# Optimization experiments

Hardware: AMD Instinct MI355X
Metric: run time of the kernel (lower is better)

The kernel has to match this reference:

```python
import jax, jax.numpy as jnp
import numpy as np

N_ITEMS = 30000
D = 128            # embedding_dim
F = D // 2 + 1     # freq_dim = 65
RAW_IMG = 1024
RAW_TXT = 768


def setup_inputs() -> dict:
    key = jax.random.key(0)
    ks = jax.random.split(key, 13)
    return {
        "image_embeds": jax.random.normal(ks[0], (N_ITEMS, D), jnp.float32),
        "text_embeds": jax.random.normal(ks[1], (N_ITEMS, D), jnp.float32),
        "image_table": jax.random.normal(ks[2], (N_ITEMS, RAW_IMG), jnp.float32),
        "text_table": jax.random.normal(ks[3], (N_ITEMS, RAW_TXT), jnp.float32),
        "W_img": jax.random.normal(ks[4], (RAW_IMG, D), jnp.float32) * 0.02,
        "b_img": jax.random.normal(ks[5], (D,), jnp.float32) * 0.02,
        "W_txt": jax.random.normal(ks[6], (RAW_TXT, D), jnp.float32) * 0.02,
        "b_txt": jax.random.normal(ks[7], (D,), jnp.float32) * 0.02,
        "avrf_img": jax.random.normal(ks[8], (F,), jnp.float32),
        "avrf_txt": jax.random.normal(ks[9], (F,), jnp.float32),
        "avg_R": jax.random.normal(ks[10], (F,), jnp.float32),
        "psi": jax.random.normal(ks[11], (F,), jnp.float32) * 0.1,
        "lambda_weights": jnp.array([0.6, 0.4], jnp.float32),
    }


def reference(image_embeds, text_embeds, image_table, text_table,
              W_img, b_img, W_txt, b_txt,
              avrf_img, avrf_txt, avg_R, psi, lambda_weights):
    # project full embedding tables: [N, raw] @ [raw, D] -> [N, D]
    proj_image = image_table @ W_img + b_img
    proj_txt = text_table @ W_txt + b_txt
    # per-row rFFT -> [N, F] complex
    img_fft = jnp.fft.rfft(proj_image, axis=1, norm="ortho")
    txt_fft = jnp.fft.rfft(proj_txt, axis=1, norm="ortho")
    # phase alignment rotation
    phi = avg_R * 0.5 + psi                      # [F]
    rot = jnp.exp(-1j * phi.astype(jnp.complex64))
    APC_img = img_fft * rot[None, :]
    APC_txt = txt_fft * jnp.conj(rot)[None, :]
    # AVRF (variance-ratio) masking -- torch forward uses the raw logit params
    img_vr = APC_img * avrf_img[None, :]
    txt_vr = APC_txt * avrf_txt[None, :]
    # IMCF: magnitude-squared coherence masking
    cross = APC_img * jnp.conj(APC_txt)
    msc = jnp.abs(cross) ** 2 / (jnp.abs(APC_img) ** 2 * jnp.abs(APC_txt) ** 2 + 1e-8)
    img_imcf = APC_img * msc
    txt_imcf = APC_txt * msc
    # softmax-weighted late fusion of the two filtered spectra
    lam = jax.nn.softmax(lambda_weights)
    img_late = lam[0] * img_vr + lam[1] * img_imcf
    txt_late = lam[0] * txt_vr + lam[1] * txt_imcf
    image_conv = jnp.fft.irfft(img_late, n=image_embeds.shape[1], axis=1, norm="ortho")
    text_conv = jnp.fft.irfft(txt_late, n=text_embeds.shape[1], axis=1, norm="ortho")
    return image_conv, text_conv
```

## Files before the change

kernel.cpp:

```cpp
#include <hip/hip_runtime.h>
#include <math.h>

typedef __bf16 bf16x8 __attribute__((ext_vector_type(8)));
typedef float f32x4 __attribute__((ext_vector_type(4)));
typedef unsigned short u16;
typedef unsigned int u32;

#define S128 0.08838834764831845f
#define TWOPI_128 0.04908738521234052f
#define MROWS 30080

__device__ __align__(16) u16 g_wft[56 * 12288];
__device__ __align__(16) u16 g_gt[6 * 8192];
__device__ __align__(16) float g_fp[96 * 8];
__device__ __align__(16) u32 g_S[(size_t)2 * 6 * 4 * MROWS * 8];

__device__ __forceinline__ void split2(float v, u16& h, u16& l) {
  unsigned u = __float_as_uint(v);
  h = (u16)(u >> 16);
  float hf = __uint_as_float(u & 0xFFFF0000u);
  float lo = v - hf;
  unsigned ul = __float_as_uint(lo);
  l = (u16)((ul + 0x7FFFu + ((ul >> 16) & 1u)) >> 16);
}

__device__ __forceinline__ void gll16(const void* gsrc, void* ldst) {
  __builtin_amdgcn_global_load_lds(
      (const __attribute__((address_space(1))) unsigned int*)gsrc,
      (__attribute__((address_space(3))) unsigned int*)ldst, 16, 0, 0);
}

__global__ void k_setup_wft(const float* __restrict__ Wimg,
                            const float* __restrict__ Wtxt, int Kimg, int Ktxt) {
  int gid = blockIdx.x * 256 + threadIdx.x;
  int imgn = Kimg * 96;
  if (gid >= imgn + Ktxt * 96) return;
  const float* Wrow;
  u16* base;
  int kloc, fq;
  if (gid < imgn) {
    kloc = gid / 96; fq = gid % 96;
    Wrow = Wimg + (size_t)kloc * 128;
    base = g_wft + (size_t)(kloc >> 5) * 12288;
  } else {
    int l = gid - imgn;
    kloc = l / 96; fq = l % 96;
    Wrow = Wtxt + (size_t)kloc * 128;
    base = g_wft + (size_t)(32 + (kloc >> 5)) * 12288;
  }
  float re = 0.f, im = 0.f;
  if (fq <= 64) {
    float sts, stc;
    sincosf(TWOPI_128 * (float)fq, &sts, &stc);
    for (int d0 = 0; d0 < 128; d0 += 16) {
      int m = (fq * d0) & 127;
      float sa, ca;
      sincosf(TWOPI_128 * (float)m, &sa, &ca);
      float cr = ca, ci = -sa;
      float wv[16];
      *(float4*)&wv[0]  = *(const float4*)&Wrow[d0];
      *(float4*)&wv[4]  = *(const float4*)&Wrow[d0 + 4];
      *(float4*)&wv[8]  = *(const float4*)&Wrow[d0 + 8];
      *(float4*)&wv[12] = *(const float4*)&Wrow[d0 + 12];
#pragma unroll
      for (int jj = 0; jj < 16; ++jj) {
        re = fmaf(wv[jj], cr, re);
        im = fmaf(wv[jj], ci, im);
        float nc = cr * stc + ci * sts;
        ci = ci * stc - cr * sts;
        cr = nc;
      }
    }
    re *= S128; im *= S128;
  }
  int gran = (kloc & 31) >> 3, j = kloc & 7;
  int cre = (fq >> 4) * 32 + (fq & 15);
  u16 h, l;
  split2(re, h, l);
  base[(gran * 1536 + cre * 8 + j) ^ (gran << 4)] = h;
  base[6144 + ((gran * 1536 + cre * 8 + j) ^ (gran << 4))] = l;
  split2(im, h, l);
  base[(gran * 1536 + (cre + 16) * 8 + j) ^ (gran << 4)] = h;
  base[6144 + ((gran * 1536 + (cre + 16) * 8 + j) ^ (gran << 4))] = l;
}

__global__ void k_setup_gt(void) {
  int gid = blockIdx.x * 256 + threadIdx.x;
  if (gid >= 192 * 128) return;
  int pk = gid >> 7, n = gid & 127;
  int ks = pk >> 5, w = pk & 31, gran = (w >> 3) & 3, j = w & 7;
  int part = w >> 4, fl = ks * 16 + (w & 15);
  float val = 0.f;
  if (fl <= 64) {
    float ck = (fl == 0 || fl == 64) ? 1.f : 2.f;
    int m = (fl * n) & 127;
    float sa, ca;
    sincosf(TWOPI_128 * (float)m, &sa, &ca);
    val = (part == 0 ? ca : -sa) * ck * S128;
  }
  u16 h, l;
  split2(val, h, l);
  g_gt[ks * 8192 + ((gran * 1024 + n * 8 + j) ^ (gran << 4))] = h;
  g_gt[ks * 8192 + 4096 + ((gran * 1024 + n * 8 + j) ^ (gran << 4))] = l;
}

__global__ void k_setup_fp(const float* __restrict__ b_img, const float* __restrict__ b_txt,
                           const float* __restrict__ avrf_img, const float* __restrict__ avrf_txt,
                           const float* __restrict__ avg_R, const float* __restrict__ psi) {
  int gid = blockIdx.x * 256 + threadIdx.x;
  if (gid >= 96 * 4) return;
  int k = gid >> 2, q = gid & 3;
  float* fp = g_fp + k * 8;
  if (k > 64) {
    if (q == 0) { fp[0] = 1.f; fp[1] = 0.f; fp[2] = 0.f; fp[3] = 0.f; }
    fp[4 + q] = 0.f;
    return;
  }
  if (q == 0) {
    float phi = avg_R[k] * 0.5f + psi[k];
    float s, c;
    sincosf(phi, &s, &c);
    fp[0] = c; fp[1] = s; fp[2] = avrf_img[k]; fp[3] = avrf_txt[k];
  }
  const float* b = (q < 2) ? b_img : b_txt;
  int part = q & 1;
  float acc = 0.f;
  for (int d = 0; d < 128; ++d) {
    int m = (k * d) & 127;
    float sa, ca;
    sincosf(TWOPI_128 * (float)m, &sa, &ca);
    acc = fmaf(b[d], part ? -sa : ca, acc);
  }
  fp[4 + q] = acc * S128;
}

__global__ __launch_bounds__(512) void k1_gemm(
    const float* __restrict__ Aimg, const float* __restrict__ Atxt,
    int M, int Kimg, int Ktxt, int bpm) {
  __shared__ __align__(16) u16 Asm[2 * 4096];
  __shared__ __align__(16) u16 Bsm[2 * 12288];

  const int bid = blockIdx.x;
  const int mod = bid >= bpm;
  const int bblk = mod ? bid - bpm : bid;
  const float* A = mod ? Atxt : Aimg;
  const int K = mod ? Ktxt : Kimg;
  const u16* wft = g_wft + (mod ? (size_t)32 * 12288 : 0);
  const int row0 = bblk * 128;

  const int tid = threadIdx.x;
  const int lane = tid & 63, wv = tid >> 6;
  const int la = lane & 15, hh = lane >> 4;
  const int wr = wv >> 1, wc = wv & 1;

  const int rseg = tid >> 2, g4 = tid & 3;
  const int awoff = (g4 * 1024 + rseg * 8) ^ (g4 << 4);
  int grow = row0 + rseg;
  if (grow > M - 1) grow = M - 1;
  const float* Abase = A + (size_t)grow * K + g4 * 8;

  f32x4 acc[2][6];
#pragma unroll
  for (int rt = 0; rt < 2; ++rt)
#pragma unroll
    for (int ct = 0; ct < 6; ++ct) acc[rt][ct] = (f32x4){0.f, 0.f, 0.f, 0.f};

  int boff[6];
#pragma unroll
  for (int ct = 0; ct < 6; ++ct)
    boff[ct] = (hh * 1536 + (wc * 96 + ct * 16 + la) * 8) ^ (hh << 4);

  const int nst = K / 32;

  auto stageB = [&](int s, int buf) {
    const u16* src = wft + (size_t)s * 12288;
    char* dst = (char*)Bsm + buf * 24576;
#pragma unroll
    for (int i = 0; i < 3; ++i)
      gll16(src + i * 4096 + tid * 8, dst + i * 8192 + tid * 16);
  };

  stageB(0, 0);
  float4 av0 = *(const float4*)(Abase);
  float4 av1 = *(const float4*)(Abase + 4);

  for (int s = 0; s < nst; ++s) {
    const int cur = s & 1;
    __syncthreads();
    {
      u16 h8[8], l8[8];
      const float va[8] = {av0.x, av0.y, av0.z, av0.w, av1.x, av1.y, av1.z, av1.w};
#pragma unroll
      for (int j = 0; j < 8; ++j) split2(va[j], h8[j], l8[j]);
      *(bf16x8*)&Asm[awoff] = *(bf16x8*)h8;
      *(bf16x8*)&Asm[4096 + awoff] = *(bf16x8*)l8;
    }
    __syncthreads();

    if (s + 1 < nst) {
      stageB(s + 1, cur ^ 1);
      av0 = *(const float4*)(Abase + (s + 1) * 32);
      av1 = *(const float4*)(Abase + (s + 1) * 32 + 4);
    }

    bf16x8 fah[2], fal[2];
#pragma unroll
    for (int rt = 0; rt < 2; ++rt) {
      const int ar = wr * 32 + rt * 16 + la;
      const int off = (hh * 1024 + ar * 8) ^ (hh << 4);
      fah[rt] = *(const bf16x8*)&Asm[off];
      fal[rt] = *(const bf16x8*)&Asm[4096 + off];
    }
    const u16* bb0 = Bsm + cur * 12288;
#pragma unroll
    for (int ct = 0; ct < 6; ++ct) {
      const bf16x8 fbh = *(const bf16x8*)&bb0[boff[ct]];
      const bf16x8 fbl = *(const bf16x8*)&bb0[6144 + boff[ct]];
#pragma unroll
      for (int rt = 0; rt < 2; ++rt) {
        acc[rt][ct] = __builtin_amdgcn_mfma_f32_16x16x32_bf16(fah[rt], fbh, acc[rt][ct], 0, 0, 0);
        acc[rt][ct] = __builtin_amdgcn_mfma_f32_16x16x32_bf16(fah[rt], fbl, acc[rt][ct], 0, 0, 0);
        acc[rt][ct] = __builtin_amdgcn_mfma_f32_16x16x32_bf16(fal[rt], fbh, acc[rt][ct], 0, 0, 0);
      }
    }
  }

#pragma unroll
  for (int ct = 0; ct < 6; ++ct) {
    const int cg = wc * 6 + ct;
    const int fq = (cg >> 1) * 16 + la;
    const float bv = g_fp[fq * 8 + 4 + mod * 2 + (cg & 1)];
    const int ks = cg >> 1;
    const int khh = (cg & 1) * 2 + (la >> 3);
    const int j8 = la & 7;
    const size_t sbase = ((size_t)((mod * 6 + ks) * 4 + khh)) * MROWS;
#pragma unroll
    for (int rt = 0; rt < 2; ++rt) {
      const int rb = row0 + wr * 32 + rt * 16 + hh * 4;
#pragma unroll
      for (int j = 0; j < 4; ++j) {
        u16 h, l;
        split2(acc[rt][ct][j] + bv, h, l);
        g_S[(sbase + rb + j) * 8 + j8] = ((u32)h << 16) | l;
      }
    }
  }
}

__global__ __launch_bounds__(256) void k2_idft(
    const float* __restrict__ lamw, float* __restrict__ out, int M) {
  __shared__ __align__(16) u16 Gs[8192];
  __shared__ __align__(16) float fps[96 * 8];

  const int tid = threadIdx.x;
  const int lane = tid & 63, wv = tid >> 6;
  const int la = lane & 15, hh = lane >> 4;
  const int part = hh >> 1;
  const int row = blockIdx.x * 64 + wv * 16 + la;

  if (tid < 192) gll16((const char*)g_fp + tid * 16, (char*)fps + tid * 16);

  const float l0 = lamw[0], l1 = lamw[1];
  const float mx = fmaxf(l0, l1);
  const float e0 = expf(l0 - mx), e1 = expf(l1 - mx);
  const float lam0 = e0 / (e0 + e1), lam1 = e1 / (e0 + e1);

  f32x4 ai[8], at[8];
#pragma unroll
  for (int ct = 0; ct < 8; ++ct) {
    ai[ct] = (f32x4){0.f, 0.f, 0.f, 0.f};
    at[ct] = (f32x4){0.f, 0.f, 0.f, 0.f};
  }

  for (int ks = 0; ks < 6; ++ks) {
    const u32* si = &g_S[((size_t)((0 + ks) * 4 + hh) * MROWS + row) * 8];
    const u32* st = &g_S[((size_t)((24 + ks * 4) + hh) * MROWS + row) * 8];
    uint4 vi0 = *(const uint4*)si, vi1 = *(const uint4*)(si + 4);
    uint4 vt0 = *(const uint4*)st, vt1 = *(const uint4*)(st + 4);

    __syncthreads();
#pragma unroll
    for (int i = 0; i < 4; ++i)
      gll16((const char*)(g_gt + ks * 8192) + i * 4096 + tid * 16,
            (char*)Gs + i * 4096 + tid * 16);
    __syncthreads();

    u32 vs_i[8], vs_t[8];
    *(uint4*)&vs_i[0] = vi0; *(uint4*)&vs_i[4] = vi1;
    *(uint4*)&vs_t[0] = vt0; *(uint4*)&vs_t[4] = vt1;

    const int fq0 = ks * 16 + (hh & 1) * 8;
    u16 yih[8], yil[8], yth[8], ytl[8];
#pragma unroll
    for (int j = 0; j < 8; ++j) {
      const f32x4 fpv = *(const f32x4*)&fps[(fq0 + j) * 8];
      const float o_i = __uint_as_float(vs_i[j] & 0xFFFF0000u) + __uint_as_float(vs_i[j] << 16);
      const float o_t = __uint_as_float(vs_t[j] & 0xFFFF0000u) + __uint_as_float(vs_t[j] << 16);
      const float p_i = __shfl_xor(o_i, 32);
      const float p_t = __shfl_xor(o_t, 32);
      const float Sre_i = part ? p_i : o_i;
      const float Sim_i = part ? o_i : p_i;
      const float Sre_t = part ? p_t : o_t;
      const float Sim_t = part ? o_t : p_t;
      const float rc = fpv[0], rs = fpv[1];
      const float Air = Sre_i * rc + Sim_i * rs, Aii = Sim_i * rc - Sre_i * rs;
      const float Atr = Sre_t * rc - Sim_t * rs, Ati = Sim_t * rc + Sre_t * rs;
      const float cre = Air * Atr + Aii * Ati, cim = Aii * Atr - Air * Ati;
      const float pa = Air * Air + Aii * Aii, pb = Atr * Atr + Ati * Ati;
      const float msc = (cre * cre + cim * cim) / (pa * pb + 1e-8f);
      const float mi = lam0 * fpv[2] + lam1 * msc;
      const float mt = lam0 * fpv[3] + lam1 * msc;
      const float yi = (part ? Aii : Air) * mi;
      const float yt = (part ? Ati : Atr) * mt;
      split2(yi, yih[j], yil[j]);
      split2(yt, yth[j], ytl[j]);
    }
    const bf16x8 fih = *(bf16x8*)yih, fil = *(bf16x8*)yil;
    const bf16x8 fth = *(bf16x8*)yth, ftl = *(bf16x8*)ytl;
#pragma unroll
    for (int ct = 0; ct < 8; ++ct) {
      const int goff = (hh * 1024 + (ct * 16 + la) * 8) ^ (hh << 4);
      const bf16x8 gh = *(const bf16x8*)&Gs[goff];
      const bf16x8 gl = *(const bf16x8*)&Gs[4096 + goff];
      ai[ct] = __builtin_amdgcn_mfma_f32_16x16x32_bf16(fih, gh, ai[ct], 0, 0, 0);
      ai[ct] = __builtin_amdgcn_mfma_f32_16x16x32_bf16(fih, gl, ai[ct], 0, 0, 0);
      ai[ct] = __builtin_amdgcn_mfma_f32_16x16x32_bf16(fil, gh, ai[ct], 0, 0, 0);
      at[ct] = __builtin_amdgcn_mfma_f32_16x16x32_bf16(fth, gh, at[ct], 0, 0, 0);
      at[ct] = __builtin_amdgcn_mfma_f32_16x16x32_bf16(fth, gl, at[ct], 0, 0, 0);
      at[ct] = __builtin_amdgcn_mfma_f32_16x16x32_bf16(ftl, gh, at[ct], 0, 0, 0);
    }
  }

  float* oimg = out;
  float* otxt = out + (size_t)M * 128;
#pragma unroll
  for (int q = 0; q < 4; ++q) {
    const int orow = blockIdx.x * 64 + wv * 16 + hh * 4 + q;
    if (orow < M) {
#pragma unroll
      for (int ct = 0; ct < 8; ++ct) {
        oimg[(size_t)orow * 128 + ct * 16 + la] = ai[ct][q];
        otxt[(size_t)orow * 128 + ct * 16 + la] = at[ct][q];
      }
    }
  }
}

extern "C" void kernel_launch(void* const* d_in, const int* in_sizes, int n_in,
                              void* d_out, int out_size, void* d_ws, size_t ws_size,
                              hipStream_t stream) {
  const float* image_table = (const float*)d_in[2];
  const float* text_table  = (const float*)d_in[3];
  const float* W_img = (const float*)d_in[4];
  const float* b_img = (const float*)d_in[5];
  const float* W_txt = (const float*)d_in[6];
  const float* b_txt = (const float*)d_in[7];
  const float* avrf_img = (const float*)d_in[8];
  const float* avrf_txt = (const float*)d_in[9];
  const float* avg_R = (const float*)d_in[10];
  const float* psi = (const float*)d_in[11];
  const float* lamw = (const float*)d_in[12];

  const int M = in_sizes[0] / 128;
  const int K_img = in_sizes[4] / 128;
  const int K_txt = in_sizes[6] / 128;

  const int wft_threads = (K_img + K_txt) * 96;
  k_setup_wft<<<(wft_threads + 255) / 256, 256, 0, stream>>>(W_img, W_txt, K_img, K_txt);
  k_setup_gt<<<(192 * 128 + 255) / 256, 256, 0, stream>>>();
  k_setup_fp<<<2, 256, 0, stream>>>(b_img, b_txt, avrf_img, avrf_txt, avg_R, psi);

  const int bpm = (M + 127) / 128;
  k1_gemm<<<2 * bpm, 512, 0, stream>>>(image_table, text_table, M, K_img, K_txt, bpm);
  k2_idft<<<(M + 63) / 64, 256, 0, stream>>>(lamw, (float*)d_out, M);
}
```

Before: 136.4 us.

## Drop low-half bf16 split for projected weights and double the K step

The fused DFT weight matrix is now stored as a single rounded bf16 value rather than a hi/lo pair, which halves the weight buffer and its staging traffic. The GEMM keeps the hi/lo split only for activations, so each K=32 chunk needs two MFMAs instead of three. Each stage now covers K=64 with a doubled A shared-memory buffer, which halves the number of loop iterations and barriers. In exchange, weight precision falls to bf16, which could raise error against the fp32 reference.

```diff
diff --git a/kernel.cpp b/kernel.cpp
--- a/kernel.cpp
+++ b/kernel.cpp
@@ -10,7 +10,7 @@
 #define TWOPI_128 0.04908738521234052f
 #define MROWS 30080
 
-__device__ __align__(16) u16 g_wft[56 * 12288];
+__device__ __align__(16) u16 g_wft[56 * 6144];
 __device__ __align__(16) u16 g_gt[6 * 8192];
 __device__ __align__(16) float g_fp[96 * 8];
 __device__ __align__(16) u32 g_S[(size_t)2 * 6 * 4 * MROWS * 8];
@@ -22,6 +22,11 @@
   float lo = v - hf;
   unsigned ul = __float_as_uint(lo);
   l = (u16)((ul + 0x7FFFu + ((ul >> 16) & 1u)) >> 16);
+}
+
+__device__ __forceinline__ u16 rne16(float v) {
+  unsigned u = __float_as_uint(v);
+  return (u16)((u + 0x7FFFu + ((u >> 16) & 1u)) >> 16);
 }
 
 __device__ __forceinline__ void gll16(const void* gsrc, void* ldst) {
@@ -41,12 +46,12 @@
   if (gid < imgn) {
     kloc = gid / 96; fq = gid % 96;
     Wrow = Wimg + (size_t)kloc * 128;
-    base = g_wft + (size_t)(kloc >> 5) * 12288;
+    base = g_wft + (size_t)(kloc >> 5) * 6144;
   } else {
     int l = gid - imgn;
     kloc = l / 96; fq = l % 96;
     Wrow = Wtxt + (size_t)kloc * 128;
-    base = g_wft + (size_t)(32 + (kloc >> 5)) * 12288;
+    base = g_wft + (size_t)(32 + (kloc >> 5)) * 6144;
   }
   float re = 0.f, im = 0.f;
   if (fq <= 64) {
@@ -75,13 +80,8 @@
   }
   int gran = (kloc & 31) >> 3, j = kloc & 7;
   int cre = (fq >> 4) * 32 + (fq & 15);
-  u16 h, l;
-  split2(re, h, l);
-  base[(gran * 1536 + cre * 8 + j) ^ (gran << 4)] = h;
-  base[6144 + ((gran * 1536 + cre * 8 + j) ^ (gran << 4))] = l;
-  split2(im, h, l);
-  base[(gran * 1536 + (cre + 16) * 8 + j) ^ (gran << 4)] = h;
-  base[6144 + ((gran * 1536 + (cre + 16) * 8 + j) ^ (gran << 4))] = l;
+  base[(gran * 1536 + cre * 8 + j) ^ (gran << 4)] = rne16(re);
+  base[(gran * 1536 + (cre + 16) * 8 + j) ^ (gran << 4)] = rne16(im);
 }
 
 __global__ void k_setup_gt(void) {
@@ -137,7 +137,7 @@
 __global__ __launch_bounds__(512) void k1_gemm(
     const float* __restrict__ Aimg, const float* __restrict__ Atxt,
     int M, int Kimg, int Ktxt, int bpm) {
-  __shared__ __align__(16) u16 Asm[2 * 4096];
+  __shared__ __align__(16) u16 Asm[2 * 8192];
   __shared__ __align__(16) u16 Bsm[2 * 12288];
 
   const int bid = blockIdx.x;
@@ -145,7 +145,7 @@
   const int bblk = mod ? bid - bpm : bid;
   const float* A = mod ? Atxt : Aimg;
   const int K = mod ? Ktxt : Kimg;
-  const u16* wft = g_wft + (mod ? (size_t)32 * 12288 : 0);
+  const u16* wft = g_wft + (mod ? (size_t)32 * 6144 : 0);
   const int row0 = bblk * 128;
 
   const int tid = threadIdx.x;
@@ -154,7 +154,8 @@
   const int wr = wv >> 1, wc = wv & 1;
 
   const int rseg = tid >> 2, g4 = tid & 3;
-  const int awoff = (g4 * 1024 + rseg * 8) ^ (g4 << 4);
+  const int aw0 = (g4 * 1024 + rseg * 8) ^ (g4 << 4);
+  const int aw1 = ((g4 + 4) * 1024 + rseg * 8) ^ (g4 << 4);
   int grow = row0 + rseg;
   if (grow > M - 1) grow = M - 1;
   const float* Abase = A + (size_t)grow * K + g4 * 8;
@@ -170,7 +171,7 @@
   for (int ct = 0; ct < 6; ++ct)
     boff[ct] = (hh * 1536 + (wc * 96 + ct * 16 + la) * 8) ^ (hh << 4);
 
-  const int nst = K / 32;
+  const int nst = K / 64;
 
   auto stageB = [&](int s, int buf) {
     const u16* src = wft + (size_t)s * 12288;
@@ -183,44 +184,62 @@
   stageB(0, 0);
   float4 av0 = *(const float4*)(Abase);
   float4 av1 = *(const float4*)(Abase + 4);
+  float4 av2 = *(const float4*)(Abase + 32);
+  float4 av3 = *(const float4*)(Abase + 36);
 
   for (int s = 0; s < nst; ++s) {
     const int cur = s & 1;
     __syncthreads();
     {
       u16 h8[8], l8[8];
-      const float va[8] = {av0.x, av0.y, av0.z, av0.w, av1.x, av1.y, av1.z, av1.w};
-#pragma unroll
-      for (int j = 0; j < 8; ++j) split2(va[j], h8[j], l8[j]);
-      *(bf16x8*)&Asm[awoff] = *(bf16x8*)h8;
-      *(bf16x8*)&Asm[4096 + awoff] = *(bf16x8*)l8;
+      {
+        const float va[8] = {av0.x, av0.y, av0.z, av0.w, av1.x, av1.y, av1.z, av1.w};
+#pragma unroll
+        for (int j = 0; j < 8; ++j) split2(va[j], h8[j], l8[j]);
+        *(bf16x8*)&Asm[aw0] = *(bf16x8*)h8;
+        *(bf16x8*)&Asm[8192 + aw0] = *(bf16x8*)l8;
+      }
+      {
+        const float va[8] = {av2.x, av2.y, av2.z, av2.w, av3.x, av3.y, av3.z, av3.w};
+#pragma unroll
+        for (int j = 0; j < 8; ++j) split2(va[j], h8[j], l8[j]);
+        *(bf16x8*)&Asm[aw1] = *(bf16x8*)h8;
+        *(bf16x8*)&Asm[8192 + aw1] = *(bf16x8*)l8;
+      }
     }
     __syncthreads();
 
     if (s + 1 < nst) {
       stageB(s + 1, cur ^ 1);
-      av0 = *(const float4*)(Abase + (s + 1) * 32);
-      av1 = *(const float4*)(Abase + (s + 1) * 32 + 4);
-    }
-
-    bf16x8 fah[2], fal[2];
+      const float* p = Abase + (s + 1) * 64;
+      av0 = *(const float4*)(p);
+      av1 = *(const float4*)(p + 4);
+      av2 = *(const float4*)(p + 32);
+      av3 = *(const float4*)(p + 36);
+    }
+
+    bf16x8 fah[2][2], fal[2][2];
 #pragma unroll
     for (int rt = 0; rt < 2; ++rt) {
       const int ar = wr * 32 + rt * 16 + la;
-      const int off = (hh * 1024 + ar * 8) ^ (hh << 4);
-      fah[rt] = *(const bf16x8*)&Asm[off];
-      fal[rt] = *(const bf16x8*)&Asm[4096 + off];
+      const int o0 = (hh * 1024 + ar * 8) ^ (hh << 4);
+      const int o1 = ((4 + hh) * 1024 + ar * 8) ^ (hh << 4);
+      fah[rt][0] = *(const bf16x8*)&Asm[o0];
+      fal[rt][0] = *(const bf16x8*)&Asm[8192 + o0];
+      fah[rt][1] = *(const bf16x8*)&Asm[o1];
+      fal[rt][1] = *(const bf16x8*)&Asm[8192 + o1];
     }
     const u16* bb0 = Bsm + cur * 12288;
 #pragma unroll
     for (int ct = 0; ct < 6; ++ct) {
-      const bf16x8 fbh = *(const bf16x8*)&bb0[boff[ct]];
-      const bf16x8 fbl = *(const bf16x8*)&bb0[6144 + boff[ct]];
+      const bf16x8 fb0 = *(const bf16x8*)&bb0[boff[ct]];
+      const bf16x8 fb1 = *(const bf16x8*)&bb0[6144 + boff[ct]];
 #pragma unroll
       for (int rt = 0; rt < 2; ++rt) {
-        acc[rt][ct] = __builtin_amdgcn_mfma_f32_16x16x32_bf16(fah[rt], fbh, acc[rt][ct], 0, 0, 0);
-        acc[rt][ct] = __builtin_amdgcn_mfma_f32_16x16x32_bf16(fah[rt], fbl, acc[rt][ct], 0, 0, 0);
-        acc[rt][ct] = __builtin_amdgcn_mfma_f32_16x16x32_bf16(fal[rt], fbh, acc[rt][ct], 0, 0, 0);
+        acc[rt][ct] = __builtin_amdgcn_mfma_f32_16x16x32_bf16(fah[rt][0], fb0, acc[rt][ct], 0, 0, 0);
+        acc[rt][ct] = __builtin_amdgcn_mfma_f32_16x16x32_bf16(fal[rt][0], fb0, acc[rt][ct], 0, 0, 0);
+        acc[rt][ct] = __builtin_amdgcn_mfma_f32_16x16x32_bf16(fah[rt][1], fb1, acc[rt][ct], 0, 0, 0);
+        acc[rt][ct] = __builtin_amdgcn_mfma_f32_16x16x32_bf16(fal[rt][1], fb1, acc[rt][ct], 0, 0, 0);
       }
     }
   }
```

Result: slower. 140.8 us (+3.2%).
